# Kernel optimization log

Measured on AMD Instinct MI355X. Metric: run time of the kernel, lower is better.

The kernel has to match this reference:

```python
import jax, jax.numpy as jnp
import numpy as np

NUM_LEVELS = 4  # -> num_components = 4*5/2 = 10 (non-recursive weights)


def _excl_cumsum(x, axis):
    # exclusive cumulative sum along `axis` (forward direction)
    return jnp.cumsum(x, axis=axis) - x


def setup_inputs() -> dict:
    key = jax.random.key(0)
    k1, k2, k3 = jax.random.split(key, 3)
    B, T, F, m = 32, 2048, 128, 64
    C = NUM_LEVELS * (NUM_LEVELS + 1) // 2  # 10
    X = jax.random.normal(k1, (B, T, F), dtype=jnp.float32)
    kernel = jax.random.normal(k2, (C, F, m), dtype=jnp.float32) / np.sqrt(F)
    bias = jax.random.normal(k3, (C, m), dtype=jnp.float32) * 0.01
    return {"X": X, "kernel": kernel, "bias": bias}


def reference(X, kernel, bias):
    # low_rank_seq2tens, embedding_order=1, recursive_weights=False,
    # reverse=False, return_sequences=False
    # M: [C, B, T, m] -- low-rank projections of the sequence for each component
    M = jnp.einsum('btf,cfm->cbtm', X, kernel) + bias[:, None, None, :]
    Y = [jnp.sum(M[0], axis=1)]  # level 1: plain time-sum, [B, m]
    k = 1
    for i in range(1, NUM_LEVELS):
        R = M[k]
        k += 1
        for _ in range(1, i + 1):
            # iterated-sum recurrence: multiply by next component's projection of
            # the exclusive prefix sum along time
            R = M[k] * _excl_cumsum(R, axis=1)
            k += 1
        Y.append(jnp.sum(R, axis=1))
    return jnp.stack(Y, axis=1)  # [B, num_levels, m]
```

## Files before the change

### kernel.cpp

```cpp
#include <hip/hip_runtime.h>
#include <hip/hip_bf16.h>
#include <stdint.h>


typedef __attribute__((ext_vector_type(8))) short short8;
typedef __attribute__((ext_vector_type(4))) float f32x4;

#define T_ 2048
#define F_ 128
#define M_ 64
#define NTILE 40
#define SEGS 32

#define VMCNT(n) asm volatile("s_waitcnt vmcnt(" #n ")" ::: "memory")

__device__ __forceinline__ unsigned short f2bf(float x){
  unsigned int u = __float_as_uint(x);
  u += 0x7FFFu + ((u>>16)&1u);
  return (unsigned short)(u>>16);
}

__device__ __forceinline__ void gl_lds16(const char* g, char* s){
  __builtin_amdgcn_global_load_lds(
    (const __attribute__((address_space(1))) unsigned int*)g,
    (__attribute__((address_space(3))) unsigned int*)s, 16, 0, 0);
}

__global__ __launch_bounds__(256) void prep_w_k(const float* __restrict__ Wk,
                                                uint4* __restrict__ wsw){
  int g = blockIdx.x*256 + threadIdx.x;
  if (g >= NTILE*4*64) return;
  int l  = g & 63;
  int kk = (g >> 6) & 3;
  int n  = g >> 8;
  int cm = n*16 + (l & 15);
  int c  = cm >> 6, mm = cm & 63;
  int kb = kk*32 + (l>>4)*8;
  unsigned short v[8];
  #pragma unroll
  for (int j=0;j<8;++j) v[j] = f2bf(Wk[((c*F_) + kb + j)*M_ + mm]);
  uint4 o;
  o.x = (unsigned)v[0] | ((unsigned)v[1]<<16);
  o.y = (unsigned)v[2] | ((unsigned)v[3]<<16);
  o.z = (unsigned)v[4] | ((unsigned)v[5]<<16);
  o.w = (unsigned)v[6] | ((unsigned)v[7]<<16);
  wsw[g] = o;
}

__device__ __forceinline__ float sx(float v, int mk){ return __shfl_xor(v, mk, 64); }

__global__ __launch_bounds__(256) void ls2t_main_k(const float* __restrict__ X,
                                                   const float* __restrict__ bias,
                                                   const char* __restrict__ wsrc,
                                                   float* __restrict__ agg){
  const int seg = blockIdx.x;
  const int b   = blockIdx.y;
  const int tid = threadIdx.x;
  const int nt  = tid >> 6;
  const int l   = tid & 63;
  const int lr  = l & 15, lg = l >> 4;
  const int t0  = seg*64;
  const int mcol = nt*16 + lr;

  __shared__ __align__(16) char xs[16384];
  __shared__ __align__(16) char wbuf[32768];

  auto stageC = [&](int c, int buf){
    const char* s = wsrc + c*16384 + nt*4096 + l*16;
    char* d = wbuf + buf*16384 + nt*4096 + l*16;
    #pragma unroll
    for (int i=0;i<4;++i) gl_lds16(s + i*1024, d + i*1024);
  };

  stageC(0,0); stageC(1,1);

  float bz[10];
  #pragma unroll
  for (int c=0;c<10;++c) bz[c] = bias[c*M_ + mcol];

  #pragma unroll
  for (int p=0;p<2;++p){
    int t  = tid & 63;
    int fp = (tid >> 6) + p*4;
    const float* src = X + ((size_t)b*T_ + t0 + t)*F_ + fp*16;
    float4 v0 = *reinterpret_cast<const float4*>(src);
    float4 v1 = *reinterpret_cast<const float4*>(src+4);
    float4 v2 = *reinterpret_cast<const float4*>(src+8);
    float4 v3 = *reinterpret_cast<const float4*>(src+12);
    uint4 q0, q1;
    q0.x = (unsigned)f2bf(v0.x) | ((unsigned)f2bf(v0.y)<<16);
    q0.y = (unsigned)f2bf(v0.z) | ((unsigned)f2bf(v0.w)<<16);
    q0.z = (unsigned)f2bf(v1.x) | ((unsigned)f2bf(v1.y)<<16);
    q0.w = (unsigned)f2bf(v1.z) | ((unsigned)f2bf(v1.w)<<16);
    q1.x = (unsigned)f2bf(v2.x) | ((unsigned)f2bf(v2.y)<<16);
    q1.y = (unsigned)f2bf(v2.z) | ((unsigned)f2bf(v2.w)<<16);
    q1.z = (unsigned)f2bf(v3.x) | ((unsigned)f2bf(v3.y)<<16);
    q1.w = (unsigned)f2bf(v3.z) | ((unsigned)f2bf(v3.w)<<16);
    int sw = (t>>2)&7;
    *reinterpret_cast<uint4*>(xs + t*256 + ((fp*2  ) ^ sw)*16) = q0;
    *reinterpret_cast<uint4*>(xs + t*256 + ((fp*2+1) ^ sw)*16) = q1;
  }
  __syncthreads();

  short8 af[4][4];
  #pragma unroll
  for (int s=0;s<4;++s)
    #pragma unroll
    for (int kk=0;kk<4;++kk)
      af[s][kk] = *reinterpret_cast<const short8*>(
          xs + (lr*4+s)*256 + (((kk*4+lg) ^ (lr&7)))*16);

  auto computeC = [&](f32x4 (&A)[4], int buf){
    const char* wb = wbuf + buf*16384 + nt*4096;
    #pragma unroll
    for (int s=0;s<4;++s) A[s] = (f32x4){0.f,0.f,0.f,0.f};
    #pragma unroll
    for (int kk=0;kk<4;++kk){
      short8 wf = *reinterpret_cast<const short8*>(wb + kk*1024 + l*16);
      #pragma unroll
      for (int s=0;s<4;++s)
        A[s] = __builtin_amdgcn_mfma_f32_16x16x32_bf16(af[s][kk], wf, A[s], 0,0,0);
    }
  };

  float* ob = agg + (((size_t)b*SEGS + seg)*20)*64 + mcol;
  f32x4 A0[4], A1[4], A2[4], A3[4];

  computeC(A0,0);
  stageC(2,0);
  {
    float S0 = 0.f;
    #pragma unroll
    for (int j=0;j<4;++j)
      #pragma unroll
      for (int s=0;s<4;++s) S0 += A0[s][j] + bz[0];
    #pragma unroll
    for (int st=0; st<2; ++st) S0 += sx(S0, 16<<st);
    if (lg==0) ob[0*64] = S0;
  }
  computeC(A0,1);
  stageC(3,1);
  VMCNT(4);
  computeC(A1,0);
  stageC(4,0);
  {
    float S1=0.f,S2=0.f,I21=0.f;
    #pragma unroll
    for (int j=0;j<4;++j)
      #pragma unroll
      for (int s=0;s<4;++s){
        float a1 = A0[s][j] + bz[1];
        float a2 = A1[s][j] + bz[2];
        I21 += a2*S1; S1 += a1; S2 += a2;
      }
    #pragma unroll
    for (int st=0; st<2; ++st){
      int mk = 16<<st; bool up = (l & mk)!=0;
      float o1=sx(S1,mk), o2=sx(S2,mk), oI=sx(I21,mk);
      float B1=up?o1:S1, B2=up?o2:S2, BI=up?oI:I21;
      float C1=up?S1:o1, C2=up?S2:o2, CI=up?I21:oI;
      S1=B1+C1; S2=B2+C2; I21=BI+CI + B1*C2;
    }
    if (lg==0) ob[1*64]=S1; else if (lg==1) ob[2*64]=S2; else if (lg==2) ob[10*64]=I21;
  }
  VMCNT(4);
  computeC(A0,1);
  stageC(5,1);
  VMCNT(4);
  computeC(A1,0);
  stageC(6,0);
  VMCNT(4);
  computeC(A2,1);
  stageC(7,1);
  {
    float S3=0.f,S4=0.f,S5=0.f,I43=0.f,I54=0.f,I543=0.f;
    #pragma unroll
    for (int j=0;j<4;++j)
      #pragma unroll
      for (int s=0;s<4;++s){
        float a3 = A0[s][j] + bz[3];
        float a4 = A1[s][j] + bz[4];
        float a5 = A2[s][j] + bz[5];
        I543 += a5*I43; I54 += a5*S4; I43 += a4*S3;
        S3 += a3; S4 += a4; S5 += a5;
      }
    #pragma unroll
    for (int st=0; st<2; ++st){
      int mk = 16<<st; bool up = (l & mk)!=0;
      float o3=sx(S3,mk), o4=sx(S4,mk), o5=sx(S5,mk);
      float oA=sx(I43,mk), oB=sx(I54,mk), oC=sx(I543,mk);
      float B3=up?o3:S3, B4=up?o4:S4, B5=up?o5:S5;
      float BA=up?oA:I43, BB=up?oB:I54, BC_=up?oC:I543;
      float C3=up?S3:o3, C4=up?S4:o4, C5=up?S5:o5;
      float CA=up?I43:oA, CB=up?I54:oB, CC=up?I543:oC;
      float n43 = BA+CA + B3*C4;
      float n54 = BB+CB + B4*C5;
      float n543= BC_+CC + BA*C5 + B3*CB;
      S3=B3+C3; S4=B4+C4; S5=B5+C5; I43=n43; I54=n54; I543=n543;
    }
    if      (lg==0){ ob[3*64]=S3;  ob[11*64]=I43; }
    else if (lg==1){ ob[4*64]=S4;  ob[12*64]=I54; }
    else if (lg==2){ ob[5*64]=S5;  ob[13*64]=I543; }
  }
  VMCNT(4);
  computeC(A0,0);
  stageC(8,0);
  VMCNT(4);
  computeC(A1,1);
  stageC(9,1);
  VMCNT(4);
  computeC(A2,0);
  VMCNT(0);
  computeC(A3,1);
  {
    float S6=0.f,S7=0.f,S8=0.f,S9=0.f;
    float I76=0.f,I87=0.f,I98=0.f,I876=0.f,I987=0.f,I9876=0.f;
    #pragma unroll
    for (int j=0;j<4;++j)
      #pragma unroll
      for (int s=0;s<4;++s){
        float a6 = A0[s][j] + bz[6];
        float a7 = A1[s][j] + bz[7];
        float a8 = A2[s][j] + bz[8];
        float a9 = A3[s][j] + bz[9];
        I9876 += a9*I876; I987 += a9*I87; I98 += a9*S8;
        I876  += a8*I76;  I87  += a8*S7;
        I76   += a7*S6;
        S6 += a6; S7 += a7; S8 += a8; S9 += a9;
      }
    #pragma unroll
    for (int st=0; st<2; ++st){
      int mk = 16<<st; bool up = (l & mk)!=0;
      float o6=sx(S6,mk), o7=sx(S7,mk), o8=sx(S8,mk), o9=sx(S9,mk);
      float oA=sx(I76,mk), oB=sx(I87,mk), oC=sx(I98,mk);
      float oD=sx(I876,mk), oE=sx(I987,mk), oF=sx(I9876,mk);
      float B6=up?o6:S6, B7=up?o7:S7, B8=up?o8:S8, B9=up?o9:S9;
      float BA=up?oA:I76, BB=up?oB:I87, BC_=up?oC:I98;
      float BD=up?oD:I876, BE=up?oE:I987, BF=up?oF:I9876;
      float C6=up?S6:o6, C7=up?S7:o7, C8=up?S8:o8, C9=up?S9:o9;
      float CA=up?I76:oA, CB=up?I87:oB, CC=up?I98:oC;
      float CD=up?I876:oD, CE=up?I987:oE, CF=up?I9876:oF;
      float n76  = BA+CA + B6*C7;
      float n87  = BB+CB + B7*C8;
      float n98  = BC_+CC + B8*C9;
      float n876 = BD+CD + BA*C8 + B6*CB;
      float n987 = BE+CE + BB*C9 + B7*CC;
      float n9876= BF+CF + BD*C9 + BA*CC + B6*CE;
      S6=B6+C6; S7=B7+C7; S8=B8+C8; S9=B9+C9;
      I76=n76; I87=n87; I98=n98; I876=n876; I987=n987; I9876=n9876;
    }
    if      (lg==0){ ob[6*64]=S6; ob[14*64]=I76; ob[18*64]=I987; }
    else if (lg==1){ ob[7*64]=S7; ob[15*64]=I87; ob[19*64]=I9876; }
    else if (lg==2){ ob[8*64]=S8; ob[16*64]=I98; }
    else           { ob[9*64]=S9; ob[17*64]=I876; }
  }
}

__device__ __forceinline__ void compose(float* A, const float* Bv){
  float n10 = A[10]+Bv[10] + A[1]*Bv[2];
  float n11 = A[11]+Bv[11] + A[3]*Bv[4];
  float n12 = A[12]+Bv[12] + A[4]*Bv[5];
  float n13 = A[13]+Bv[13] + A[11]*Bv[5] + A[3]*Bv[12];
  float n14 = A[14]+Bv[14] + A[6]*Bv[7];
  float n15 = A[15]+Bv[15] + A[7]*Bv[8];
  float n16 = A[16]+Bv[16] + A[8]*Bv[9];
  float n17 = A[17]+Bv[17] + A[14]*Bv[8] + A[6]*Bv[15];
  float n18 = A[18]+Bv[18] + A[15]*Bv[9] + A[7]*Bv[16];
  float n19 = A[19]+Bv[19] + A[17]*Bv[9] + A[14]*Bv[16] + A[6]*Bv[18];
  #pragma unroll
  for (int c=0;c<10;++c) A[c] += Bv[c];
  A[10]=n10; A[11]=n11; A[12]=n12; A[13]=n13; A[14]=n14;
  A[15]=n15; A[16]=n16; A[17]=n17; A[18]=n18; A[19]=n19;
}

__global__ __launch_bounds__(256) void combine_k(const float* __restrict__ agg,
                                                 float* __restrict__ out){
  int b  = blockIdx.x;
  int m  = threadIdx.x & 63;
  int sg = threadIdx.x >> 6;
  const float* base = agg + ((size_t)b*SEGS*20)*64 + m;
  float st[20];
  #pragma unroll
  for (int i=0;i<20;++i) st[i]=0.f;
  #pragma unroll 2
  for (int s=sg*8; s<sg*8+8; ++s){
    const float* a = base + (size_t)s*20*64;
    float Bv[20];
    #pragma unroll
    for (int i=0;i<20;++i) Bv[i] = a[i*64];
    compose(st, Bv);
  }
  __shared__ float buf[4][20][64];
  #pragma unroll
  for (int i=0;i<20;++i) buf[sg][i][m] = st[i];
  __syncthreads();
  if (sg==0){
    #pragma unroll
    for (int g=1; g<4; ++g){
      float Bv[20];
      #pragma unroll
      for (int i=0;i<20;++i) Bv[i] = buf[g][i][m];
      compose(st, Bv);
    }
    out[(b*4+0)*64+m] = st[0];
    out[(b*4+1)*64+m] = st[10];
    out[(b*4+2)*64+m] = st[13];
    out[(b*4+3)*64+m] = st[19];
  }
}

extern "C" void kernel_launch(void* const* d_in, const int* in_sizes, int n_in,
                              void* d_out, int out_size, void* d_ws, size_t ws_size,
                              hipStream_t stream){
  const float* X    = (const float*)d_in[0];
  const float* Wk   = (const float*)d_in[1];
  const float* bias = (const float*)d_in[2];
  float* out = (float*)d_out;

  uint4* wsw = (uint4*)d_ws;
  float* agg = (float*)((char*)d_ws + (1u<<20));

  hipLaunchKernelGGL(prep_w_k,    dim3(40),     dim3(256), 0, stream, Wk, wsw);
  hipLaunchKernelGGL(ls2t_main_k, dim3(32,32),  dim3(256), 0, stream,
                     X, bias, (const char*)d_ws, agg);
  hipLaunchKernelGGL(combine_k,   dim3(32),     dim3(256), 0, stream, agg, out);
}
```

Baseline: 35.57 us.

## Drop in-wave shuffle composition, emit per-lane-group partials, alias LDS buffers

The main kernel no longer composes the 16-row lane groups with cross-lane shuffles. Each lane group now writes its own partial state, so there are 128 segments per batch instead of 32. The x-tile LDS area is reused as one of the two weight buffers, which halves shared memory (48KB to 32KB) to allow more resident blocks, at the cost of an extra barrier and less prefetch depth at the start. Bias is folded into the MFMA accumulator init, and the combine kernel grows to 512 threads to compose the four times larger partial array, which adds global traffic.

```diff
diff --git a/kernel.cpp b/kernel.cpp
--- a/kernel.cpp
+++ b/kernel.cpp
@@ -10,9 +10,10 @@
 #define F_ 128
 #define M_ 64
 #define NTILE 40
-#define SEGS 32
-
-#define VMCNT(n) asm volatile("s_waitcnt vmcnt(" #n ")" ::: "memory")
+#define SEGS2 128
+
+#define VMCNT4 asm volatile("s_waitcnt vmcnt(4)" ::: "memory")
+#define VMCNT0 asm volatile("s_waitcnt vmcnt(0)" ::: "memory")
 
 __device__ __forceinline__ unsigned short f2bf(float x){
   unsigned int u = __float_as_uint(x);
@@ -46,8 +47,6 @@
   o.w = (unsigned)v[6] | ((unsigned)v[7]<<16);
   wsw[g] = o;
 }
-
-__device__ __forceinline__ float sx(float v, int mk){ return __shfl_xor(v, mk, 64); }
 
 __global__ __launch_bounds__(256) void ls2t_main_k(const float* __restrict__ X,
                                                    const float* __restrict__ bias,
@@ -62,17 +61,17 @@
   const int t0  = seg*64;
   const int mcol = nt*16 + lr;
 
-  __shared__ __align__(16) char xs[16384];
-  __shared__ __align__(16) char wbuf[32768];
-
-  auto stageC = [&](int c, int buf){
+  __shared__ __align__(16) char smem[32768];
+  char* xs = smem;
+
+  auto stageC = [&](int c, int half){
     const char* s = wsrc + c*16384 + nt*4096 + l*16;
-    char* d = wbuf + buf*16384 + nt*4096 + l*16;
+    char* d = smem + (half ? 0 : 16384) + nt*4096 + l*16;
     #pragma unroll
     for (int i=0;i<4;++i) gl_lds16(s + i*1024, d + i*1024);
   };
 
-  stageC(0,0); stageC(1,1);
+  stageC(0,0);
 
   float bz[10];
   #pragma unroll
@@ -110,10 +109,13 @@
       af[s][kk] = *reinterpret_cast<const short8*>(
           xs + (lr*4+s)*256 + (((kk*4+lg) ^ (lr&7)))*16);
 
-  auto computeC = [&](f32x4 (&A)[4], int buf){
-    const char* wb = wbuf + buf*16384 + nt*4096;
-    #pragma unroll
-    for (int s=0;s<4;++s) A[s] = (f32x4){0.f,0.f,0.f,0.f};
+  __syncthreads();
+  stageC(1,1);
+
+  auto computeC = [&](f32x4 (&A)[4], int half, float bzc){
+    const char* wb = smem + (half ? 0 : 16384) + nt*4096;
+    #pragma unroll
+    for (int s=0;s<4;++s) A[s] = (f32x4){bzc,bzc,bzc,bzc};
     #pragma unroll
     for (int kk=0;kk<4;++kk){
       short8 wf = *reinterpret_cast<const short8*>(wb + kk*1024 + l*16);
@@ -123,25 +125,24 @@
     }
   };
 
-  float* ob = agg + (((size_t)b*SEGS + seg)*20)*64 + mcol;
-  f32x4 A0[4], A1[4], A2[4], A3[4];
-
-  computeC(A0,0);
+  float* ob = agg + ((size_t)(b*SEGS2 + seg*4 + lg)*20)*64 + mcol;
+  f32x4 GA[4], GB[4], GC[4], GD[4];
+
+  computeC(GA,0,bz[0]);
   stageC(2,0);
   {
     float S0 = 0.f;
     #pragma unroll
     for (int j=0;j<4;++j)
       #pragma unroll
-      for (int s=0;s<4;++s) S0 += A0[s][j] + bz[0];
-    #pragma unroll
-    for (int st=0; st<2; ++st) S0 += sx(S0, 16<<st);
-    if (lg==0) ob[0*64] = S0;
-  }
-  computeC(A0,1);
+      for (int s=0;s<4;++s) S0 += GA[s][j];
+    ob[0*64] = S0;
+  }
+  VMCNT4;
+  computeC(GA,1,bz[1]);
   stageC(3,1);
-  VMCNT(4);
-  computeC(A1,0);
+  VMCNT4;
+  computeC(GB,0,bz[2]);
   stageC(4,0);
   {
     float S1=0.f,S2=0.f,I21=0.f;
@@ -149,28 +150,19 @@
     for (int j=0;j<4;++j)
       #pragma unroll
       for (int s=0;s<4;++s){
-        float a1 = A0[s][j] + bz[1];
-        float a2 = A1[s][j] + bz[2];
+        float a1 = GA[s][j], a2 = GB[s][j];
         I21 += a2*S1; S1 += a1; S2 += a2;
       }
-    #pragma unroll
-    for (int st=0; st<2; ++st){
-      int mk = 16<<st; bool up = (l & mk)!=0;
-      float o1=sx(S1,mk), o2=sx(S2,mk), oI=sx(I21,mk);
-      float B1=up?o1:S1, B2=up?o2:S2, BI=up?oI:I21;
-      float C1=up?S1:o1, C2=up?S2:o2, CI=up?I21:oI;
-      S1=B1+C1; S2=B2+C2; I21=BI+CI + B1*C2;
-    }
-    if (lg==0) ob[1*64]=S1; else if (lg==1) ob[2*64]=S2; else if (lg==2) ob[10*64]=I21;
-  }
-  VMCNT(4);
-  computeC(A0,1);
+    ob[1*64]=S1; ob[2*64]=S2; ob[10*64]=I21;
+  }
+  VMCNT4;
+  computeC(GA,1,bz[3]);
   stageC(5,1);
-  VMCNT(4);
-  computeC(A1,0);
+  VMCNT4;
+  computeC(GB,0,bz[4]);
   stageC(6,0);
-  VMCNT(4);
-  computeC(A2,1);
+  VMCNT4;
+  computeC(GC,1,bz[5]);
   stageC(7,1);
   {
     float S3=0.f,S4=0.f,S5=0.f,I43=0.f,I54=0.f,I543=0.f;
@@ -178,40 +170,23 @@
     for (int j=0;j<4;++j)
       #pragma unroll
       for (int s=0;s<4;++s){
-        float a3 = A0[s][j] + bz[3];
-        float a4 = A1[s][j] + bz[4];
-        float a5 = A2[s][j] + bz[5];
+        float a3 = GA[s][j], a4 = GB[s][j], a5 = GC[s][j];
         I543 += a5*I43; I54 += a5*S4; I43 += a4*S3;
         S3 += a3; S4 += a4; S5 += a5;
       }
-    #pragma unroll
-    for (int st=0; st<2; ++st){
-      int mk = 16<<st; bool up = (l & mk)!=0;
-      float o3=sx(S3,mk), o4=sx(S4,mk), o5=sx(S5,mk);
-      float oA=sx(I43,mk), oB=sx(I54,mk), oC=sx(I543,mk);
-      float B3=up?o3:S3, B4=up?o4:S4, B5=up?o5:S5;
-      float BA=up?oA:I43, BB=up?oB:I54, BC_=up?oC:I543;
-      float C3=up?S3:o3, C4=up?S4:o4, C5=up?S5:o5;
-      float CA=up?I43:oA, CB=up?I54:oB, CC=up?I543:oC;
-      float n43 = BA+CA + B3*C4;
-      float n54 = BB+CB + B4*C5;
-      float n543= BC_+CC + BA*C5 + B3*CB;
-      S3=B3+C3; S4=B4+C4; S5=B5+C5; I43=n43; I54=n54; I543=n543;
-    }
-    if      (lg==0){ ob[3*64]=S3;  ob[11*64]=I43; }
-    else if (lg==1){ ob[4*64]=S4;  ob[12*64]=I54; }
-    else if (lg==2){ ob[5*64]=S5;  ob[13*64]=I543; }
-  }
-  VMCNT(4);
-  computeC(A0,0);
+    ob[3*64]=S3; ob[4*64]=S4; ob[5*64]=S5;
+    ob[11*64]=I43; ob[12*64]=I54; ob[13*64]=I543;
+  }
+  VMCNT4;
+  computeC(GA,0,bz[6]);
   stageC(8,0);
-  VMCNT(4);
-  computeC(A1,1);
+  VMCNT4;
+  computeC(GB,1,bz[7]);
   stageC(9,1);
-  VMCNT(4);
-  computeC(A2,0);
-  VMCNT(0);
-  computeC(A3,1);
+  VMCNT4;
+  computeC(GC,0,bz[8]);
+  VMCNT0;
+  computeC(GD,1,bz[9]);
   {
     float S6=0.f,S7=0.f,S8=0.f,S9=0.f;
     float I76=0.f,I87=0.f,I98=0.f,I876=0.f,I987=0.f,I9876=0.f;
@@ -219,40 +194,15 @@
     for (int j=0;j<4;++j)
       #pragma unroll
       for (int s=0;s<4;++s){
-        float a6 = A0[s][j] + bz[6];
-        float a7 = A1[s][j] + bz[7];
-        float a8 = A2[s][j] + bz[8];
-        float a9 = A3[s][j] + bz[9];
+        float a6 = GA[s][j], a7 = GB[s][j], a8 = GC[s][j], a9 = GD[s][j];
         I9876 += a9*I876; I987 += a9*I87; I98 += a9*S8;
         I876  += a8*I76;  I87  += a8*S7;
         I76   += a7*S6;
         S6 += a6; S7 += a7; S8 += a8; S9 += a9;
       }
-    #pragma unroll
-    for (int st=0; st<2; ++st){
-      int mk = 16<<st; bool up = (l & mk)!=0;
-      float o6=sx(S6,mk), o7=sx(S7,mk), o8=sx(S8,mk), o9=sx(S9,mk);
-      float oA=sx(I76,mk), oB=sx(I87,mk), oC=sx(I98,mk);
-      float oD=sx(I876,mk), oE=sx(I987,mk), oF=sx(I9876,mk);
-      float B6=up?o6:S6, B7=up?o7:S7, B8=up?o8:S8, B9=up?o9:S9;
-      float BA=up?oA:I76, BB=up?oB:I87, BC_=up?oC:I98;
-      float BD=up?oD:I876, BE=up?oE:I987, BF=up?oF:I9876;
-      float C6=up?S6:o6, C7=up?S7:o7, C8=up?S8:o8, C9=up?S9:o9;
-      float CA=up?I76:oA, CB=up?I87:oB, CC=up?I98:oC;
-      float CD=up?I876:oD, CE=up?I987:oE, CF=up?I9876:oF;
-      float n76  = BA+CA + B6*C7;
-      float n87  = BB+CB + B7*C8;
-      float n98  = BC_+CC + B8*C9;
-      float n876 = BD+CD + BA*C8 + B6*CB;
-      float n987 = BE+CE + BB*C9 + B7*CC;
-      float n9876= BF+CF + BD*C9 + BA*CC + B6*CE;
-      S6=B6+C6; S7=B7+C7; S8=B8+C8; S9=B9+C9;
-      I76=n76; I87=n87; I98=n98; I876=n876; I987=n987; I9876=n9876;
-    }
-    if      (lg==0){ ob[6*64]=S6; ob[14*64]=I76; ob[18*64]=I987; }
-    else if (lg==1){ ob[7*64]=S7; ob[15*64]=I87; ob[19*64]=I9876; }
-    else if (lg==2){ ob[8*64]=S8; ob[16*64]=I98; }
-    else           { ob[9*64]=S9; ob[17*64]=I876; }
+    ob[6*64]=S6; ob[7*64]=S7; ob[8*64]=S8; ob[9*64]=S9;
+    ob[14*64]=I76; ob[15*64]=I87; ob[16*64]=I98;
+    ob[17*64]=I876; ob[18*64]=I987; ob[19*64]=I9876;
   }
 }
 
@@ -273,30 +223,29 @@
   A[15]=n15; A[16]=n16; A[17]=n17; A[18]=n18; A[19]=n19;
 }
 
-__global__ __launch_bounds__(256) void combine_k(const float* __restrict__ agg,
+__global__ __launch_bounds__(512) void combine_k(const float* __restrict__ agg,
                                                  float* __restrict__ out){
   int b  = blockIdx.x;
   int m  = threadIdx.x & 63;
   int sg = threadIdx.x >> 6;
-  const float* base = agg + ((size_t)b*SEGS*20)*64 + m;
+  const float* base = agg + ((size_t)b*SEGS2*20)*64 + m;
   float st[20];
   #pragma unroll
   for (int i=0;i<20;++i) st[i]=0.f;
-  #pragma unroll 2
-  for (int s=sg*8; s<sg*8+8; ++s){
+  for (int s=sg*16; s<sg*16+16; ++s){
     const float* a = base + (size_t)s*20*64;
     float Bv[20];
     #pragma unroll
     for (int i=0;i<20;++i) Bv[i] = a[i*64];
     compose(st, Bv);
   }
-  __shared__ float buf[4][20][64];
+  __shared__ float buf[8][20][64];
   #pragma unroll
   for (int i=0;i<20;++i) buf[sg][i][m] = st[i];
   __syncthreads();
   if (sg==0){
     #pragma unroll
-    for (int g=1; g<4; ++g){
+    for (int g=1; g<8; ++g){
       float Bv[20];
       #pragma unroll
       for (int i=0;i<20;++i) Bv[i] = buf[g][i][m];
@@ -323,5 +272,5 @@
   hipLaunchKernelGGL(prep_w_k,    dim3(40),     dim3(256), 0, stream, Wk, wsw);
   hipLaunchKernelGGL(ls2t_main_k, dim3(32,32),  dim3(256), 0, stream,
                      X, bias, (const char*)d_ws, agg);
-  hipLaunchKernelGGL(combine_k,   dim3(32),     dim3(256), 0, stream, agg, out);
-}
+  hipLaunchKernelGGL(combine_k,   dim3(32),     dim3(512), 0, stream, agg, out);
+}
```

New measurement: 37.97 us. +6.7%, slower.

## Process two time segments per block sharing staged weight tiles in LDS

Applied to the files above, without the earlier changes.

Each block now has 512 threads covering two adjacent 64-step segments, and both wave groups share each staged weight tile, each group loading half of it. Weights rotate through a four-slot LDS ring with explicit vmcnt waits and barriers, and the bias is folded into the MFMA accumulator initialisation. The aim is to halve weight staging traffic per segment and deepen prefetch. In exchange it adds a block-wide barrier before every component and leaves fewer, larger blocks with 64KB of LDS each.

```diff
diff --git a/kernel.cpp b/kernel.cpp
--- a/kernel.cpp
+++ b/kernel.cpp
@@ -12,7 +12,10 @@
 #define NTILE 40
 #define SEGS 32
 
-#define VMCNT(n) asm volatile("s_waitcnt vmcnt(" #n ")" ::: "memory")
+#define VMCNT4 asm volatile("s_waitcnt vmcnt(4)" ::: "memory")
+#define VMCNT2 asm volatile("s_waitcnt vmcnt(2)" ::: "memory")
+#define VMCNT0 asm volatile("s_waitcnt vmcnt(0)" ::: "memory")
+#define BAR    __builtin_amdgcn_s_barrier()
 
 __device__ __forceinline__ unsigned short f2bf(float x){
   unsigned int u = __float_as_uint(x);
@@ -49,56 +52,63 @@
 
 __device__ __forceinline__ float sx(float v, int mk){ return __shfl_xor(v, mk, 64); }
 
-__global__ __launch_bounds__(256) void ls2t_main_k(const float* __restrict__ X,
+__global__ __launch_bounds__(512) void ls2t_main_k(const float* __restrict__ X,
                                                    const float* __restrict__ bias,
                                                    const char* __restrict__ wsrc,
                                                    float* __restrict__ agg){
-  const int seg = blockIdx.x;
-  const int b   = blockIdx.y;
-  const int tid = threadIdx.x;
-  const int nt  = tid >> 6;
-  const int l   = tid & 63;
-  const int lr  = l & 15, lg = l >> 4;
-  const int t0  = seg*64;
+  const int pair = blockIdx.x;
+  const int b    = blockIdx.y;
+  const int tid  = threadIdx.x;
+  const int w    = tid >> 6;
+  const int tg   = w >> 2;
+  const int nt   = w & 3;
+  const int l    = tid & 63;
+  const int lr   = l & 15, lg = l >> 4;
+  const int seg  = pair*2 + tg;
+  const int t0   = seg*64;
   const int mcol = nt*16 + lr;
 
-  __shared__ __align__(16) char xs[16384];
-  __shared__ __align__(16) char wbuf[32768];
-
-  auto stageC = [&](int c, int buf){
-    const char* s = wsrc + c*16384 + nt*4096 + l*16;
-    char* d = wbuf + buf*16384 + nt*4096 + l*16;
-    #pragma unroll
-    for (int i=0;i<4;++i) gl_lds16(s + i*1024, d + i*1024);
+  __shared__ __align__(16) char smem[65536];
+  static const int WOFF[4] = {32768, 0, 16384, 49152};
+
+  auto stageC = [&](int c, int off){
+    const char* s = wsrc + c*16384 + nt*4096 + tg*2048 + l*16;
+    char* d = smem + off + nt*4096 + tg*2048 + l*16;
+    gl_lds16(s,        d);
+    gl_lds16(s + 1024, d + 1024);
   };
 
-  stageC(0,0); stageC(1,1);
+  stageC(0, WOFF[0]);
 
   float bz[10];
   #pragma unroll
   for (int c=0;c<10;++c) bz[c] = bias[c*M_ + mcol];
 
-  #pragma unroll
-  for (int p=0;p<2;++p){
-    int t  = tid & 63;
-    int fp = (tid >> 6) + p*4;
-    const float* src = X + ((size_t)b*T_ + t0 + t)*F_ + fp*16;
-    float4 v0 = *reinterpret_cast<const float4*>(src);
-    float4 v1 = *reinterpret_cast<const float4*>(src+4);
-    float4 v2 = *reinterpret_cast<const float4*>(src+8);
-    float4 v3 = *reinterpret_cast<const float4*>(src+12);
-    uint4 q0, q1;
-    q0.x = (unsigned)f2bf(v0.x) | ((unsigned)f2bf(v0.y)<<16);
-    q0.y = (unsigned)f2bf(v0.z) | ((unsigned)f2bf(v0.w)<<16);
-    q0.z = (unsigned)f2bf(v1.x) | ((unsigned)f2bf(v1.y)<<16);
-    q0.w = (unsigned)f2bf(v1.z) | ((unsigned)f2bf(v1.w)<<16);
-    q1.x = (unsigned)f2bf(v2.x) | ((unsigned)f2bf(v2.y)<<16);
-    q1.y = (unsigned)f2bf(v2.z) | ((unsigned)f2bf(v2.w)<<16);
-    q1.z = (unsigned)f2bf(v3.x) | ((unsigned)f2bf(v3.y)<<16);
-    q1.w = (unsigned)f2bf(v3.z) | ((unsigned)f2bf(v3.w)<<16);
-    int sw = (t>>2)&7;
-    *reinterpret_cast<uint4*>(xs + t*256 + ((fp*2  ) ^ sw)*16) = q0;
-    *reinterpret_cast<uint4*>(xs + t*256 + ((fp*2+1) ^ sw)*16) = q1;
+  char* xs = smem + tg*16384;
+  {
+    int t2 = tid & 255;
+    #pragma unroll
+    for (int p=0;p<2;++p){
+      int t  = t2 & 63;
+      int fp = (t2 >> 6) + p*4;
+      const float* src = X + ((size_t)b*T_ + t0 + t)*F_ + fp*16;
+      float4 v0 = *reinterpret_cast<const float4*>(src);
+      float4 v1 = *reinterpret_cast<const float4*>(src+4);
+      float4 v2 = *reinterpret_cast<const float4*>(src+8);
+      float4 v3 = *reinterpret_cast<const float4*>(src+12);
+      uint4 q0, q1;
+      q0.x = (unsigned)f2bf(v0.x) | ((unsigned)f2bf(v0.y)<<16);
+      q0.y = (unsigned)f2bf(v0.z) | ((unsigned)f2bf(v0.w)<<16);
+      q0.z = (unsigned)f2bf(v1.x) | ((unsigned)f2bf(v1.y)<<16);
+      q0.w = (unsigned)f2bf(v1.z) | ((unsigned)f2bf(v1.w)<<16);
+      q1.x = (unsigned)f2bf(v2.x) | ((unsigned)f2bf(v2.y)<<16);
+      q1.y = (unsigned)f2bf(v2.z) | ((unsigned)f2bf(v2.w)<<16);
+      q1.z = (unsigned)f2bf(v3.x) | ((unsigned)f2bf(v3.y)<<16);
+      q1.w = (unsigned)f2bf(v3.z) | ((unsigned)f2bf(v3.w)<<16);
+      int sw = (t>>2)&7;
+      *reinterpret_cast<uint4*>(xs + t*256 + ((fp*2  ) ^ sw)*16) = q0;
+      *reinterpret_cast<uint4*>(xs + t*256 + ((fp*2+1) ^ sw)*16) = q1;
+    }
   }
   __syncthreads();
 
@@ -109,11 +119,16 @@
     for (int kk=0;kk<4;++kk)
       af[s][kk] = *reinterpret_cast<const short8*>(
           xs + (lr*4+s)*256 + (((kk*4+lg) ^ (lr&7)))*16);
-
-  auto computeC = [&](f32x4 (&A)[4], int buf){
-    const char* wb = wbuf + buf*16384 + nt*4096;
-    #pragma unroll
-    for (int s=0;s<4;++s) A[s] = (f32x4){0.f,0.f,0.f,0.f};
+  asm volatile("s_waitcnt lgkmcnt(0)" ::: "memory");
+  __builtin_amdgcn_sched_barrier(0);
+  BAR;
+  stageC(1, WOFF[1]);
+  stageC(2, WOFF[2]);
+
+  auto computeC = [&](f32x4 (&A)[4], int off, float bzc){
+    const char* wb = smem + off + nt*4096;
+    #pragma unroll
+    for (int s=0;s<4;++s) A[s] = (f32x4){bzc,bzc,bzc,bzc};
     #pragma unroll
     for (int kk=0;kk<4;++kk){
       short8 wf = *reinterpret_cast<const short8*>(wb + kk*1024 + l*16);
@@ -124,33 +139,33 @@
   };
 
   float* ob = agg + (((size_t)b*SEGS + seg)*20)*64 + mcol;
-  f32x4 A0[4], A1[4], A2[4], A3[4];
-
-  computeC(A0,0);
-  stageC(2,0);
+  f32x4 GA[4], GB[4], GC[4], GD[4];
+
+  computeC(GA, WOFF[0], bz[0]);
+  stageC(3, WOFF[3]);
   {
     float S0 = 0.f;
     #pragma unroll
     for (int j=0;j<4;++j)
       #pragma unroll
-      for (int s=0;s<4;++s) S0 += A0[s][j] + bz[0];
+      for (int s=0;s<4;++s) S0 += GA[s][j];
     #pragma unroll
     for (int st=0; st<2; ++st) S0 += sx(S0, 16<<st);
     if (lg==0) ob[0*64] = S0;
   }
-  computeC(A0,1);
-  stageC(3,1);
-  VMCNT(4);
-  computeC(A1,0);
-  stageC(4,0);
+  VMCNT4; BAR;
+  computeC(GA, WOFF[1], bz[1]);
+  stageC(4, WOFF[0]);
+  VMCNT4; BAR;
+  computeC(GB, WOFF[2], bz[2]);
+  stageC(5, WOFF[1]);
   {
     float S1=0.f,S2=0.f,I21=0.f;
     #pragma unroll
     for (int j=0;j<4;++j)
       #pragma unroll
       for (int s=0;s<4;++s){
-        float a1 = A0[s][j] + bz[1];
-        float a2 = A1[s][j] + bz[2];
+        float a1 = GA[s][j], a2 = GB[s][j];
         I21 += a2*S1; S1 += a1; S2 += a2;
       }
     #pragma unroll
@@ -163,24 +178,22 @@
     }
     if (lg==0) ob[1*64]=S1; else if (lg==1) ob[2*64]=S2; else if (lg==2) ob[10*64]=I21;
   }
-  VMCNT(4);
-  computeC(A0,1);
-  stageC(5,1);
-  VMCNT(4);
-  computeC(A1,0);
-  stageC(6,0);
-  VMCNT(4);
-  computeC(A2,1);
-  stageC(7,1);
+  VMCNT4; BAR;
+  computeC(GA, WOFF[3], bz[3]);
+  stageC(6, WOFF[2]);
+  VMCNT4; BAR;
+  computeC(GB, WOFF[0], bz[4]);
+  stageC(7, WOFF[3]);
+  VMCNT4; BAR;
+  computeC(GC, WOFF[1], bz[5]);
+  stageC(8, WOFF[0]);
   {
     float S3=0.f,S4=0.f,S5=0.f,I43=0.f,I54=0.f,I543=0.f;
     #pragma unroll
     for (int j=0;j<4;++j)
       #pragma unroll
       for (int s=0;s<4;++s){
-        float a3 = A0[s][j] + bz[3];
-        float a4 = A1[s][j] + bz[4];
-        float a5 = A2[s][j] + bz[5];
+        float a3 = GA[s][j], a4 = GB[s][j], a5 = GC[s][j];
         I543 += a5*I43; I54 += a5*S4; I43 += a4*S3;
         S3 += a3; S4 += a4; S5 += a5;
       }
@@ -202,16 +215,15 @@
     else if (lg==1){ ob[4*64]=S4;  ob[12*64]=I54; }
     else if (lg==2){ ob[5*64]=S5;  ob[13*64]=I543; }
   }
-  VMCNT(4);
-  computeC(A0,0);
-  stageC(8,0);
-  VMCNT(4);
-  computeC(A1,1);
-  stageC(9,1);
-  VMCNT(4);
-  computeC(A2,0);
-  VMCNT(0);
-  computeC(A3,1);
+  VMCNT4; BAR;
+  computeC(GA, WOFF[2], bz[6]);
+  stageC(9, WOFF[1]);
+  VMCNT4; BAR;
+  computeC(GB, WOFF[3], bz[7]);
+  VMCNT2; BAR;
+  computeC(GC, WOFF[0], bz[8]);
+  VMCNT0; BAR;
+  computeC(GD, WOFF[1], bz[9]);
   {
     float S6=0.f,S7=0.f,S8=0.f,S9=0.f;
     float I76=0.f,I87=0.f,I98=0.f,I876=0.f,I987=0.f,I9876=0.f;
@@ -219,10 +231,7 @@
     for (int j=0;j<4;++j)
       #pragma unroll
       for (int s=0;s<4;++s){
-        float a6 = A0[s][j] + bz[6];
-        float a7 = A1[s][j] + bz[7];
-        float a8 = A2[s][j] + bz[8];
-        float a9 = A3[s][j] + bz[9];
+        float a6 = GA[s][j], a7 = GB[s][j], a8 = GC[s][j], a9 = GD[s][j];
         I9876 += a9*I876; I987 += a9*I87; I98 += a9*S8;
         I876  += a8*I76;  I87  += a8*S7;
         I76   += a7*S6;
@@ -321,7 +330,7 @@
   float* agg = (float*)((char*)d_ws + (1u<<20));
 
   hipLaunchKernelGGL(prep_w_k,    dim3(40),     dim3(256), 0, stream, Wk, wsw);
-  hipLaunchKernelGGL(ls2t_main_k, dim3(32,32),  dim3(256), 0, stream,
+  hipLaunchKernelGGL(ls2t_main_k, dim3(16,32),  dim3(512), 0, stream,
                      X, bias, (const char*)d_ws, agg);
   hipLaunchKernelGGL(combine_k,   dim3(32),     dim3(256), 0, stream, agg, out);
 }
```

Measured after the change: 35.97 us. Within noise of the previous version (+1.1%).

## Load MFMA operands directly into registers instead of staging through LDS

Applied to the files above, without the earlier changes.

Removes the LDS staging of X and weight tiles. Each lane now loads its X fragment straight from global memory into registers and converts it to bf16, and the weight fragments are double-buffered in registers with asm anchors that order each prefetch after the previous compute. Bias is folded into the MFMA accumulator's initial value, and launch bounds request 2 blocks per SM. This drops the LDS writes and reads, the __syncthreads and the manual vmcnt waits. In exchange it raises register pressure and relies on uncoalesced per-lane global reads of X.

```diff
diff --git a/kernel.cpp b/kernel.cpp
--- a/kernel.cpp
+++ b/kernel.cpp
@@ -12,18 +12,13 @@
 #define NTILE 40
 #define SEGS 32
 
-#define VMCNT(n) asm volatile("s_waitcnt vmcnt(" #n ")" ::: "memory")
-
 __device__ __forceinline__ unsigned short f2bf(float x){
   unsigned int u = __float_as_uint(x);
   u += 0x7FFFu + ((u>>16)&1u);
   return (unsigned short)(u>>16);
 }
-
-__device__ __forceinline__ void gl_lds16(const char* g, char* s){
-  __builtin_amdgcn_global_load_lds(
-    (const __attribute__((address_space(1))) unsigned int*)g,
-    (__attribute__((address_space(3))) unsigned int*)s, 16, 0, 0);
+__device__ __forceinline__ unsigned pk2(float lo, float hi){
+  return (unsigned)f2bf(lo) | ((unsigned)f2bf(hi)<<16);
 }
 
 __global__ __launch_bounds__(256) void prep_w_k(const float* __restrict__ Wk,
@@ -49,10 +44,10 @@
 
 __device__ __forceinline__ float sx(float v, int mk){ return __shfl_xor(v, mk, 64); }
 
-__global__ __launch_bounds__(256) void ls2t_main_k(const float* __restrict__ X,
-                                                   const float* __restrict__ bias,
-                                                   const char* __restrict__ wsrc,
-                                                   float* __restrict__ agg){
+__global__ __launch_bounds__(256, 2) void ls2t_main_k(const float* __restrict__ X,
+                                                      const float* __restrict__ bias,
+                                                      const uint4* __restrict__ wfrag,
+                                                      float* __restrict__ agg){
   const int seg = blockIdx.x;
   const int b   = blockIdx.y;
   const int tid = threadIdx.x;
@@ -62,95 +57,79 @@
   const int t0  = seg*64;
   const int mcol = nt*16 + lr;
 
-  __shared__ __align__(16) char xs[16384];
-  __shared__ __align__(16) char wbuf[32768];
-
-  auto stageC = [&](int c, int buf){
-    const char* s = wsrc + c*16384 + nt*4096 + l*16;
-    char* d = wbuf + buf*16384 + nt*4096 + l*16;
-    #pragma unroll
-    for (int i=0;i<4;++i) gl_lds16(s + i*1024, d + i*1024);
+  short8 af[4][4];
+  #pragma unroll
+  for (int s=0;s<4;++s){
+    const float* xr = X + ((size_t)b*T_ + t0 + lr*4 + s)*F_ + lg*8;
+    #pragma unroll
+    for (int kk=0;kk<4;++kk){
+      float4 v0 = *reinterpret_cast<const float4*>(xr + kk*32);
+      float4 v1 = *reinterpret_cast<const float4*>(xr + kk*32 + 4);
+      uint4 q;
+      q.x = pk2(v0.x, v0.y);
+      q.y = pk2(v0.z, v0.w);
+      q.z = pk2(v1.x, v1.y);
+      q.w = pk2(v1.z, v1.w);
+      af[s][kk] = reinterpret_cast<short8&>(q);
+    }
+  }
+
+  float bz[10];
+  #pragma unroll
+  for (int c=0;c<10;++c) bz[c] = bias[c*M_ + mcol];
+
+  auto wld0 = [&](int c, uint4 (&W)[4]){
+    #pragma unroll
+    for (int kk=0;kk<4;++kk) W[kk] = wfrag[(size_t)(((c*4+nt)*4)+kk)*64 + l];
   };
-
-  stageC(0,0); stageC(1,1);
-
-  float bz[10];
-  #pragma unroll
-  for (int c=0;c<10;++c) bz[c] = bias[c*M_ + mcol];
-
-  #pragma unroll
-  for (int p=0;p<2;++p){
-    int t  = tid & 63;
-    int fp = (tid >> 6) + p*4;
-    const float* src = X + ((size_t)b*T_ + t0 + t)*F_ + fp*16;
-    float4 v0 = *reinterpret_cast<const float4*>(src);
-    float4 v1 = *reinterpret_cast<const float4*>(src+4);
-    float4 v2 = *reinterpret_cast<const float4*>(src+8);
-    float4 v3 = *reinterpret_cast<const float4*>(src+12);
-    uint4 q0, q1;
-    q0.x = (unsigned)f2bf(v0.x) | ((unsigned)f2bf(v0.y)<<16);
-    q0.y = (unsigned)f2bf(v0.z) | ((unsigned)f2bf(v0.w)<<16);
-    q0.z = (unsigned)f2bf(v1.x) | ((unsigned)f2bf(v1.y)<<16);
-    q0.w = (unsigned)f2bf(v1.z) | ((unsigned)f2bf(v1.w)<<16);
-    q1.x = (unsigned)f2bf(v2.x) | ((unsigned)f2bf(v2.y)<<16);
-    q1.y = (unsigned)f2bf(v2.z) | ((unsigned)f2bf(v2.w)<<16);
-    q1.z = (unsigned)f2bf(v3.x) | ((unsigned)f2bf(v3.y)<<16);
-    q1.w = (unsigned)f2bf(v3.z) | ((unsigned)f2bf(v3.w)<<16);
-    int sw = (t>>2)&7;
-    *reinterpret_cast<uint4*>(xs + t*256 + ((fp*2  ) ^ sw)*16) = q0;
-    *reinterpret_cast<uint4*>(xs + t*256 + ((fp*2+1) ^ sw)*16) = q1;
-  }
-  __syncthreads();
-
-  short8 af[4][4];
-  #pragma unroll
-  for (int s=0;s<4;++s)
-    #pragma unroll
-    for (int kk=0;kk<4;++kk)
-      af[s][kk] = *reinterpret_cast<const short8*>(
-          xs + (lr*4+s)*256 + (((kk*4+lg) ^ (lr&7)))*16);
-
-  auto computeC = [&](f32x4 (&A)[4], int buf){
-    const char* wb = wbuf + buf*16384 + nt*4096;
-    #pragma unroll
-    for (int s=0;s<4;++s) A[s] = (f32x4){0.f,0.f,0.f,0.f};
+  auto wld = [&](int c, uint4 (&W)[4], float anchor){
+    const uint4* p = wfrag + (size_t)((c*4+nt)*4)*64 + l;
+    asm volatile("" : "+v"(p) : "v"(anchor));
+    #pragma unroll
+    for (int kk=0;kk<4;++kk) W[kk] = p[(size_t)kk*64];
+  };
+  auto cmp = [&](f32x4 (&A)[4], const uint4 (&W)[4], float bzc){
+    #pragma unroll
+    for (int s=0;s<4;++s) A[s] = (f32x4){bzc,bzc,bzc,bzc};
     #pragma unroll
     for (int kk=0;kk<4;++kk){
-      short8 wf = *reinterpret_cast<const short8*>(wb + kk*1024 + l*16);
+      short8 wf = reinterpret_cast<const short8&>(W[kk]);
       #pragma unroll
       for (int s=0;s<4;++s)
         A[s] = __builtin_amdgcn_mfma_f32_16x16x32_bf16(af[s][kk], wf, A[s], 0,0,0);
     }
   };
 
+  uint4 Wa[4], Wb[4];
+  wld0(0, Wa);
+  wld0(1, Wb);
+
   float* ob = agg + (((size_t)b*SEGS + seg)*20)*64 + mcol;
-  f32x4 A0[4], A1[4], A2[4], A3[4];
-
-  computeC(A0,0);
-  stageC(2,0);
+  f32x4 GA[4], GB[4], GC[4], GD[4];
+
+  cmp(GA, Wa, bz[0]);
+  wld(2, Wa, GA[0][0]);
   {
     float S0 = 0.f;
     #pragma unroll
     for (int j=0;j<4;++j)
       #pragma unroll
-      for (int s=0;s<4;++s) S0 += A0[s][j] + bz[0];
+      for (int s=0;s<4;++s) S0 += GA[s][j];
     #pragma unroll
     for (int st=0; st<2; ++st) S0 += sx(S0, 16<<st);
     if (lg==0) ob[0*64] = S0;
   }
-  computeC(A0,1);
-  stageC(3,1);
-  VMCNT(4);
-  computeC(A1,0);
-  stageC(4,0);
+  cmp(GA, Wb, bz[1]);
+  wld(3, Wb, GA[0][0]);
+  cmp(GB, Wa, bz[2]);
+  wld(4, Wa, GB[0][0]);
   {
     float S1=0.f,S2=0.f,I21=0.f;
     #pragma unroll
     for (int j=0;j<4;++j)
       #pragma unroll
       for (int s=0;s<4;++s){
-        float a1 = A0[s][j] + bz[1];
-        float a2 = A1[s][j] + bz[2];
+        float a1 = GA[s][j], a2 = GB[s][j];
         I21 += a2*S1; S1 += a1; S2 += a2;
       }
     #pragma unroll
@@ -163,24 +142,19 @@
     }
     if (lg==0) ob[1*64]=S1; else if (lg==1) ob[2*64]=S2; else if (lg==2) ob[10*64]=I21;
   }
-  VMCNT(4);
-  computeC(A0,1);
-  stageC(5,1);
-  VMCNT(4);
-  computeC(A1,0);
-  stageC(6,0);
-  VMCNT(4);
-  computeC(A2,1);
-  stageC(7,1);
+  cmp(GA, Wb, bz[3]);
+  wld(5, Wb, GA[0][0]);
+  cmp(GB, Wa, bz[4]);
+  wld(6, Wa, GB[0][0]);
+  cmp(GC, Wb, bz[5]);
+  wld(7, Wb, GC[0][0]);
   {
     float S3=0.f,S4=0.f,S5=0.f,I43=0.f,I54=0.f,I543=0.f;
     #pragma unroll
     for (int j=0;j<4;++j)
       #pragma unroll
       for (int s=0;s<4;++s){
-        float a3 = A0[s][j] + bz[3];
-        float a4 = A1[s][j] + bz[4];
-        float a5 = A2[s][j] + bz[5];
+        float a3 = GA[s][j], a4 = GB[s][j], a5 = GC[s][j];
         I543 += a5*I43; I54 += a5*S4; I43 += a4*S3;
         S3 += a3; S4 += a4; S5 += a5;
       }
@@ -202,16 +176,12 @@
     else if (lg==1){ ob[4*64]=S4;  ob[12*64]=I54; }
     else if (lg==2){ ob[5*64]=S5;  ob[13*64]=I543; }
   }
-  VMCNT(4);
-  computeC(A0,0);
-  stageC(8,0);
-  VMCNT(4);
-  computeC(A1,1);
-  stageC(9,1);
-  VMCNT(4);
-  computeC(A2,0);
-  VMCNT(0);
-  computeC(A3,1);
+  cmp(GA, Wa, bz[6]);
+  wld(8, Wa, GA[0][0]);
+  cmp(GB, Wb, bz[7]);
+  wld(9, Wb, GB[0][0]);
+  cmp(GC, Wa, bz[8]);
+  cmp(GD, Wb, bz[9]);
   {
     float S6=0.f,S7=0.f,S8=0.f,S9=0.f;
     float I76=0.f,I87=0.f,I98=0.f,I876=0.f,I987=0.f,I9876=0.f;
@@ -219,10 +189,7 @@
     for (int j=0;j<4;++j)
       #pragma unroll
       for (int s=0;s<4;++s){
-        float a6 = A0[s][j] + bz[6];
-        float a7 = A1[s][j] + bz[7];
-        float a8 = A2[s][j] + bz[8];
-        float a9 = A3[s][j] + bz[9];
+        float a6 = GA[s][j], a7 = GB[s][j], a8 = GC[s][j], a9 = GD[s][j];
         I9876 += a9*I876; I987 += a9*I87; I98 += a9*S8;
         I876  += a8*I76;  I87  += a8*S7;
         I76   += a7*S6;
@@ -322,6 +289,6 @@
 
   hipLaunchKernelGGL(prep_w_k,    dim3(40),     dim3(256), 0, stream, Wk, wsw);
   hipLaunchKernelGGL(ls2t_main_k, dim3(32,32),  dim3(256), 0, stream,
-                     X, bias, (const char*)d_ws, agg);
+                     X, bias, (const uint4*)d_ws, agg);
   hipLaunchKernelGGL(combine_k,   dim3(32),     dim3(256), 0, stream, agg, out);
 }
```

Measured after the change: 42.86 us. 1.2x slower.
